# Performance work log

Measured on AMD Instinct MI355X. Metric: run time of the kernel, lower is better.

## Reference

```python
import jax, jax.numpy as jnp
import numpy as np

B, N, D, ATT = 8, 2048, 1024, 128

def setup_inputs() -> dict:
    key = jax.random.key(0)
    k1, k2, k3 = jax.random.split(key, 3)
    s = 1.0 / np.sqrt(D)
    return {
        "x": jax.random.normal(k1, (B, N, D), dtype=jnp.float32),
        "Wf": jax.random.normal(k2, (D, ATT), dtype=jnp.float32) * s,
        "bf": jnp.zeros((ATT,), dtype=jnp.float32),
        "Wg": jax.random.normal(k3, (D, ATT), dtype=jnp.float32) * s,
        "bg": jnp.zeros((ATT,), dtype=jnp.float32),
    }

def reference(x, Wf, bf, Wg, bg):
    # f, g: [B, N, ATT]
    f = jnp.einsum('bnd,da->bna', x, Wf) + bf
    g = jnp.einsum('bnd,da->bna', x, Wg) + bg
    # unscaled attention logits [B, N, N]
    att = jnp.einsum('bna,bma->bnm', f, g)
    att = jax.nn.softmax(att, axis=-1)
    # NOTE: original multiplies attention with x (not h); h branch is dead code.
    out = jnp.einsum('bnm,bmd->bnd', att, x)
    return out + x  # residual=True
```

## Files before the change

kernel.cpp:

```cpp
#include <hip/hip_runtime.h>
#include <hip/hip_fp16.h>


#define B_ 8
#define N_ 2048
#define D_ 1024
#define A_ 128

typedef _Float16 half8v  __attribute__((ext_vector_type(8)));
typedef _Float16 half4v  __attribute__((ext_vector_type(4)));
typedef float    floatx4 __attribute__((ext_vector_type(4)));

__device__ __forceinline__ floatx4 mfma32(half8v a, half8v b, floatx4 c) {
#if defined(__HIP_DEVICE_COMPILE__)
    return __builtin_amdgcn_mfma_f32_16x16x32_f16(a, b, c, 0, 0, 0);
#else
    return c;
#endif
}

__global__ __launch_bounds__(256) void xpose_kernel(
    const float* __restrict__ x, _Float16* __restrict__ xT)
{
    __shared__ __align__(16) _Float16 ts[64][80];
    const int n0 = blockIdx.x * 64, d0 = blockIdx.y * 64, b = blockIdx.z;
    const int t = threadIdx.x;
#pragma unroll
    for (int s = 0; s < 4; ++s) {
        int idx = t + 256 * s;
        int nl = idx >> 4, c4 = idx & 15;
        float4 v = ((const float4*)(x + ((size_t)(b * N_ + n0 + nl)) * D_ + d0))[c4];
        ts[c4 * 4 + 0][nl] = (_Float16)v.x;
        ts[c4 * 4 + 1][nl] = (_Float16)v.y;
        ts[c4 * 4 + 2][nl] = (_Float16)v.z;
        ts[c4 * 4 + 3][nl] = (_Float16)v.w;
    }
    __syncthreads();
#pragma unroll
    for (int s = 0; s < 2; ++s) {
        int idx = t + 256 * s;
        int dl = idx >> 3, c = idx & 7;
        *(uint4*)&xT[((size_t)b * D_ + d0 + dl) * N_ + n0 + c * 8] =
            *(const uint4*)&ts[dl][c * 8];
    }
}

__global__ __launch_bounds__(256) void wprep_kernel(
    const float* __restrict__ Wf, const float* __restrict__ Wg,
    _Float16* __restrict__ whT)
{
    __shared__ __align__(16) _Float16 ts[64][72];
    const int k0 = blockIdx.x * 64, c0 = blockIdx.y * 64;
    const float* W = blockIdx.z ? Wg : Wf;
    _Float16* dst = whT + (size_t)blockIdx.z * A_ * D_;
    const int t = threadIdx.x;
#pragma unroll
    for (int s = 0; s < 4; ++s) {
        int idx = t + 256 * s;
        int kl = idx >> 4, c4 = idx & 15;
        float4 v = *(const float4*)&W[(size_t)(k0 + kl) * A_ + c0 + c4 * 4];
        ts[c4 * 4 + 0][kl] = (_Float16)v.x;
        ts[c4 * 4 + 1][kl] = (_Float16)v.y;
        ts[c4 * 4 + 2][kl] = (_Float16)v.z;
        ts[c4 * 4 + 3][kl] = (_Float16)v.w;
    }
    __syncthreads();
#pragma unroll
    for (int s = 0; s < 2; ++s) {
        int idx = t + 256 * s;
        int cl = idx >> 3, ch = idx & 7;
        *(uint4*)&dst[(size_t)(c0 + cl) * D_ + k0 + ch * 8] =
            *(const uint4*)&ts[cl][ch * 8];
    }
}

__global__ __launch_bounds__(256) void fgmm_kernel(
    const float* __restrict__ x, const _Float16* __restrict__ whT,
    const float* __restrict__ bfv, const float* __restrict__ bgv,
    _Float16* __restrict__ fh, _Float16* __restrict__ gh)
{
    __shared__ __align__(16) _Float16 xs[64 * 40];
    __shared__ __align__(16) _Float16 wt[256 * 40];
    const int row0 = blockIdx.x * 64;
    const int t = threadIdx.x;
    const int w = t >> 6, lane = t & 63, quad = lane >> 4, l16 = lane & 15;
    const int wr  = (w >> 1) * 32;
    const int wch = (w & 1);

    float4 xRf[2];
    uint4  wR[4];
#define FG_LOAD_TILE(K0)                                                      \
    {                                                                         \
        _Pragma("unroll")                                                     \
        for (int s = 0; s < 2; ++s) {                                         \
            int idx = t + 256 * s;                                            \
            int r = idx >> 3, k4 = idx & 7;                                   \
            xRf[s] = *(const float4*)&x[(size_t)(row0 + r) * D_ + (K0) + k4 * 4]; \
        }                                                                     \
        _Pragma("unroll")                                                     \
        for (int s = 0; s < 4; ++s) {                                         \
            int idx = t + 256 * s;                                            \
            int c = idx >> 2, k8 = idx & 3;                                   \
            wR[s] = *(const uint4*)&whT[(size_t)c * D_ + (K0) + k8 * 8];      \
        }                                                                     \
    }

    FG_LOAD_TILE(0)

    floatx4 acc[2][8];
#pragma unroll
    for (int ms = 0; ms < 2; ++ms)
#pragma unroll
        for (int nt = 0; nt < 8; ++nt)
            acc[ms][nt] = (floatx4){0.f, 0.f, 0.f, 0.f};

    for (int kt = 0; kt < 32; ++kt) {
        __syncthreads();
#pragma unroll
        for (int s = 0; s < 2; ++s) {
            int idx = t + 256 * s;
            int r = idx >> 3, k4 = idx & 7;
            half4v h = {(_Float16)xRf[s].x, (_Float16)xRf[s].y,
                        (_Float16)xRf[s].z, (_Float16)xRf[s].w};
            *(half4v*)&xs[r * 40 + k4 * 4] = h;
        }
#pragma unroll
        for (int s = 0; s < 4; ++s) {
            int idx = t + 256 * s;
            int c = idx >> 2, k8 = idx & 3;
            *(uint4*)&wt[c * 40 + k8 * 8] = wR[s];
        }
        __syncthreads();
        if (kt < 31) FG_LOAD_TILE((kt + 1) * 32)

        half8v a0 = *(const half8v*)&xs[(wr + l16) * 40 + quad * 8];
        half8v a1 = *(const half8v*)&xs[(wr + 16 + l16) * 40 + quad * 8];
#pragma unroll
        for (int nt = 0; nt < 8; ++nt) {
            half8v bfr = *(const half8v*)&wt[(wch * 128 + nt * 16 + l16) * 40 + quad * 8];
            acc[0][nt] = mfma32(a0, bfr, acc[0][nt]);
            acc[1][nt] = mfma32(a1, bfr, acc[1][nt]);
        }
    }

    _Float16* dst = wch ? gh : fh;
    const float* bias = wch ? bgv : bfv;
#pragma unroll
    for (int nt = 0; nt < 8; ++nt) {
        int col = nt * 16 + l16;
        float bv = bias[col];
#pragma unroll
        for (int ms = 0; ms < 2; ++ms)
#pragma unroll
            for (int rg = 0; rg < 4; ++rg) {
                int row = row0 + wr + ms * 16 + quad * 4 + rg;
                dst[(size_t)row * A_ + col] = (_Float16)(acc[ms][nt][rg] + bv);
            }
    }
}

__global__ __launch_bounds__(256, 2) void attn_kernel(
    const float* __restrict__ x, const _Float16* __restrict__ f,
    const _Float16* __restrict__ g, const _Float16* __restrict__ xT,
    float* __restrict__ out)
{
    __shared__ __align__(16) _Float16 gS[2][32 * 136];
    __shared__ __align__(16) _Float16 xTs[2][256 * 40];

    const int dch = blockIdx.x;
    const int nt  = blockIdx.y;
    const int b   = blockIdx.z;
    const int tid = threadIdx.x;
    const int wave = tid >> 6, lane = tid & 63;
    const int quad = lane >> 4, l16 = lane & 15;
    const int d0 = dch * 256;
    const int qbase = nt * 128 + wave * 32;

    half8v fb[2][4];
#pragma unroll
    for (int it = 0; it < 2; ++it)
#pragma unroll
        for (int kc = 0; kc < 4; ++kc)
            fb[it][kc] = *(const half8v*)(f +
                ((size_t)(b * N_ + qbase + it * 16 + l16)) * A_ + kc * 32 + quad * 8);

    uint4 gR[2];
    uint2 xR[8];
#define AT_LOAD_TILE(M0)                                                      \
    {                                                                         \
        _Pragma("unroll")                                                     \
        for (int s = 0; s < 2; ++s) {                                         \
            int idx = tid + 256 * s;                                          \
            int r = idx >> 4, c = idx & 15;                                   \
            gR[s] = *(const uint4*)(g + ((size_t)(b * N_ + (M0) + r)) * A_ + c * 8); \
        }                                                                     \
        _Pragma("unroll")                                                     \
        for (int s = 0; s < 8; ++s) {                                         \
            int idx = tid + 256 * s;                                          \
            int rr = idx >> 3, p = idx & 7;                                   \
            xR[s] = *(const uint2*)(xT + ((size_t)b * D_ + d0 + rr) * N_ + (M0) + p * 4); \
        }                                                                     \
    }

#define AT_COMMIT(BUF)                                                        \
    {                                                                         \
        _Pragma("unroll")                                                     \
        for (int s = 0; s < 2; ++s) {                                         \
            int idx = tid + 256 * s;                                          \
            int r = idx >> 4, c = idx & 15;                                   \
            int slot = ((r >> 2) & 1) * 16 + ((r >> 3) & 3) * 4 + (r & 3);    \
            *(uint4*)&gS[BUF][slot * 136 + c * 8] = gR[s];                    \
        }                                                                     \
        _Pragma("unroll")                                                     \
        for (int s = 0; s < 8; ++s) {                                         \
            int idx = tid + 256 * s;                                          \
            int rr = idx >> 3, p = idx & 7;                                   \
            *(uint2*)&xTs[BUF][rr * 40 + p * 4] = xR[s];                      \
        }                                                                     \
    }

    floatx4 acc[2][16];
#pragma unroll
    for (int it = 0; it < 2; ++it)
#pragma unroll
        for (int dt = 0; dt < 16; ++dt)
            acc[it][dt] = (floatx4){0.f, 0.f, 0.f, 0.f};
    float m_i[2]    = {-3.0e38f, -3.0e38f};
    float l_part[2] = {0.f, 0.f};

    AT_LOAD_TILE(0)
    AT_COMMIT(0)
    __syncthreads();
    AT_LOAD_TILE(32)

    for (int t = 0; t < 64; ++t) {
        const int cur = t & 1;
        if (t < 63) AT_COMMIT(cur ^ 1)
        if (t < 62) AT_LOAD_TILE((t + 2) * 32)

        floatx4 sc[2][2];
#pragma unroll
        for (int fr = 0; fr < 2; ++fr)
#pragma unroll
            for (int it = 0; it < 2; ++it)
                sc[fr][it] = (floatx4){0.f, 0.f, 0.f, 0.f};
        __builtin_amdgcn_s_setprio(1);
#pragma unroll
        for (int kc = 0; kc < 4; ++kc) {
            half8v ga0 = *(const half8v*)&gS[cur][(l16     ) * 136 + kc * 32 + quad * 8];
            half8v ga1 = *(const half8v*)&gS[cur][(l16 + 16) * 136 + kc * 32 + quad * 8];
            sc[0][0] = mfma32(ga0, fb[0][kc], sc[0][0]);
            sc[0][1] = mfma32(ga0, fb[1][kc], sc[0][1]);
            sc[1][0] = mfma32(ga1, fb[0][kc], sc[1][0]);
            sc[1][1] = mfma32(ga1, fb[1][kc], sc[1][1]);
        }
        __builtin_amdgcn_s_setprio(0);

        float tm[2];
#pragma unroll
        for (int it = 0; it < 2; ++it) {
            float t0 = fmaxf(fmaxf(sc[0][it][0], sc[0][it][1]),
                             fmaxf(sc[0][it][2], sc[0][it][3]));
            float t1 = fmaxf(fmaxf(sc[1][it][0], sc[1][it][1]),
                             fmaxf(sc[1][it][2], sc[1][it][3]));
            float tv = fmaxf(t0, t1);
            tv = fmaxf(tv, __shfl_xor(tv, 16));
            tv = fmaxf(tv, __shfl_xor(tv, 32));
            tm[it] = tv;
        }
        bool needl = (tm[0] > m_i[0] + 8.0f) || (tm[1] > m_i[1] + 8.0f);
        if (__any(needl)) {
            float alpha[2];
#pragma unroll
            for (int it = 0; it < 2; ++it) {
                float mnew = fmaxf(m_i[it], tm[it]);
                alpha[it] = __expf(m_i[it] - mnew);
                m_i[it] = mnew;
                l_part[it] *= alpha[it];
            }
            float ar[2][4];
#pragma unroll
            for (int it = 0; it < 2; ++it)
#pragma unroll
                for (int r = 0; r < 4; ++r)
                    ar[it][r] = __shfl(alpha[it], quad * 4 + r);
#pragma unroll
            for (int it = 0; it < 2; ++it)
#pragma unroll
                for (int dt = 0; dt < 16; ++dt)
#pragma unroll
                    for (int r = 0; r < 4; ++r)
                        acc[it][dt][r] *= ar[it][r];
        }

        half8v pa[2];
#pragma unroll
        for (int it = 0; it < 2; ++it) {
            float e0 = __expf(sc[0][it][0] - m_i[it]);
            float e1 = __expf(sc[0][it][1] - m_i[it]);
            float e2 = __expf(sc[0][it][2] - m_i[it]);
            float e3 = __expf(sc[0][it][3] - m_i[it]);
            float e4 = __expf(sc[1][it][0] - m_i[it]);
            float e5 = __expf(sc[1][it][1] - m_i[it]);
            float e6 = __expf(sc[1][it][2] - m_i[it]);
            float e7 = __expf(sc[1][it][3] - m_i[it]);
            l_part[it] += ((e0 + e1) + (e2 + e3)) + ((e4 + e5) + (e6 + e7));
            pa[it] = (half8v){(_Float16)e0, (_Float16)e1, (_Float16)e2,
                              (_Float16)e3, (_Float16)e4, (_Float16)e5,
                              (_Float16)e6, (_Float16)e7};
        }

        __builtin_amdgcn_s_setprio(1);
#pragma unroll
        for (int dt = 0; dt < 16; ++dt) {
            half8v xb = *(const half8v*)&xTs[cur][(dt * 16 + l16) * 40 + quad * 8];
            acc[0][dt] = mfma32(pa[0], xb, acc[0][dt]);
            acc[1][dt] = mfma32(pa[1], xb, acc[1][dt]);
        }
        __builtin_amdgcn_s_setprio(0);

        __syncthreads();
    }

    float l_i[2];
#pragma unroll
    for (int it = 0; it < 2; ++it) {
        float rs = l_part[it];
        rs += __shfl_xor(rs, 16);
        rs += __shfl_xor(rs, 32);
        l_i[it] = rs;
    }
    float linv[2][4];
#pragma unroll
    for (int it = 0; it < 2; ++it)
#pragma unroll
        for (int r = 0; r < 4; ++r)
            linv[it][r] = 1.0f / __shfl(l_i[it], quad * 4 + r);

#pragma unroll
    for (int it = 0; it < 2; ++it)
#pragma unroll
        for (int r = 0; r < 4; ++r) {
            const size_t rowoff =
                ((size_t)(b * N_ + qbase + it * 16 + quad * 4 + r)) * D_ + d0;
#pragma unroll
            for (int dt = 0; dt < 16; ++dt) {
                int col = dt * 16 + l16;
                out[rowoff + col] = fmaf(acc[it][dt][r], linv[it][r], x[rowoff + col]);
            }
        }
}

extern "C" void kernel_launch(void* const* d_in, const int* in_sizes, int n_in,
                              void* d_out, int out_size, void* d_ws, size_t ws_size,
                              hipStream_t stream) {
    const float* x   = (const float*)d_in[0];
    const float* Wf  = (const float*)d_in[1];
    const float* bfv = (const float*)d_in[2];
    const float* Wg  = (const float*)d_in[3];
    const float* bgv = (const float*)d_in[4];
    float* out = (float*)d_out;

    _Float16* fh  = (_Float16*)d_ws;
    _Float16* gh  = fh + (size_t)B_ * N_ * A_;
    _Float16* xT  = gh + (size_t)B_ * N_ * A_;
    _Float16* whT = xT + (size_t)B_ * D_ * N_;

    hipLaunchKernelGGL(xpose_kernel, dim3(N_ / 64, D_ / 64, B_), dim3(256), 0, stream,
                       x, xT);
    hipLaunchKernelGGL(wprep_kernel, dim3(D_ / 64, A_ / 64, 2), dim3(256), 0, stream,
                       Wf, Wg, whT);
    hipLaunchKernelGGL(fgmm_kernel, dim3(B_ * N_ / 64), dim3(256), 0, stream,
                       x, whT, bfv, bgv, fh, gh);
    hipLaunchKernelGGL(attn_kernel, dim3(D_ / 256, N_ / 128, B_), dim3(256), 0, stream,
                       x, fh, gh, xT, out);
}
```

Measured before the change: 310.9 us.

## Stage attention tiles via direct global-to-LDS loads and halve d-chunk width

Replaces the register-staged global loads and LDS commits in the attention kernel with global_load_lds direct copies, and uses an XOR swizzle on the g tile in place of padding to avoid bank conflicts. The d-chunk per block shrinks from 256 to 128, which halves accumulators and raises occupancy to 3 blocks per CU. The cost is that the QK^T scores and softmax are recomputed twice as many times across d-chunks, and prefetch depth drops to one tile ahead.

```diff
diff --git a/kernel.cpp b/kernel.cpp
--- a/kernel.cpp
+++ b/kernel.cpp
@@ -16,6 +16,14 @@
     return __builtin_amdgcn_mfma_f32_16x16x32_f16(a, b, c, 0, 0, 0);
 #else
     return c;
+#endif
+}
+
+__device__ __forceinline__ void gload_lds16(const void* gsrc, void* ldst) {
+#if defined(__HIP_DEVICE_COMPILE__)
+    __builtin_amdgcn_global_load_lds(
+        (const __attribute__((address_space(1))) void*)gsrc,
+        (__attribute__((address_space(3))) void*)ldst, 16, 0, 0);
 #endif
 }
 
@@ -159,13 +167,13 @@
     }
 }
 
-__global__ __launch_bounds__(256, 2) void attn_kernel(
+__global__ __launch_bounds__(256, 3) void attn_kernel(
     const float* __restrict__ x, const _Float16* __restrict__ f,
     const _Float16* __restrict__ g, const _Float16* __restrict__ xT,
     float* __restrict__ out)
 {
-    __shared__ __align__(16) _Float16 gS[2][32 * 136];
-    __shared__ __align__(16) _Float16 xTs[2][256 * 40];
+    __shared__ __align__(16) _Float16 gS[2][32 * 128];
+    __shared__ __align__(16) _Float16 xTs[2][128 * 32];
 
     const int dch = blockIdx.x;
     const int nt  = blockIdx.y;
@@ -173,7 +181,7 @@
     const int tid = threadIdx.x;
     const int wave = tid >> 6, lane = tid & 63;
     const int quad = lane >> 4, l16 = lane & 15;
-    const int d0 = dch * 256;
+    const int d0 = dch * 128;
     const int qbase = nt * 128 + wave * 32;
 
     half8v fb[2][4];
@@ -184,59 +192,41 @@
             fb[it][kc] = *(const half8v*)(f +
                 ((size_t)(b * N_ + qbase + it * 16 + l16)) * A_ + kc * 32 + quad * 8);
 
-    uint4 gR[2];
-    uint2 xR[8];
-#define AT_LOAD_TILE(M0)                                                      \
+#define AT_STAGE(BUF, M0)                                                     \
     {                                                                         \
         _Pragma("unroll")                                                     \
         for (int s = 0; s < 2; ++s) {                                         \
-            int idx = tid + 256 * s;                                          \
-            int r = idx >> 4, c = idx & 15;                                   \
-            gR[s] = *(const uint4*)(g + ((size_t)(b * N_ + (M0) + r)) * A_ + c * 8); \
+            int idx = s * 256 + tid;                                          \
+            int rsl = idx >> 4, c = idx & 15;                                 \
+            int j  = ((rsl >> 2) & 3) * 8 + ((rsl >> 4) & 1) * 4 + (rsl & 3); \
+            int cc = c ^ (rsl & 7);                                           \
+            gload_lds16(g + ((size_t)(b * N_ + (M0) + j)) * A_ + cc * 8,      \
+                        &gS[BUF][(s * 256 + wave * 64) * 8]);                 \
         }                                                                     \
         _Pragma("unroll")                                                     \
-        for (int s = 0; s < 8; ++s) {                                         \
-            int idx = tid + 256 * s;                                          \
-            int rr = idx >> 3, p = idx & 7;                                   \
-            xR[s] = *(const uint2*)(xT + ((size_t)b * D_ + d0 + rr) * N_ + (M0) + p * 4); \
+        for (int s = 0; s < 2; ++s) {                                         \
+            int idx = s * 256 + tid;                                          \
+            int rr = idx >> 2, p = idx & 3;                                   \
+            gload_lds16(xT + ((size_t)b * D_ + d0 + rr) * N_ + (M0) + p * 8,  \
+                        &xTs[BUF][(s * 256 + wave * 64) * 8]);                \
         }                                                                     \
     }
 
-#define AT_COMMIT(BUF)                                                        \
-    {                                                                         \
-        _Pragma("unroll")                                                     \
-        for (int s = 0; s < 2; ++s) {                                         \
-            int idx = tid + 256 * s;                                          \
-            int r = idx >> 4, c = idx & 15;                                   \
-            int slot = ((r >> 2) & 1) * 16 + ((r >> 3) & 3) * 4 + (r & 3);    \
-            *(uint4*)&gS[BUF][slot * 136 + c * 8] = gR[s];                    \
-        }                                                                     \
-        _Pragma("unroll")                                                     \
-        for (int s = 0; s < 8; ++s) {                                         \
-            int idx = tid + 256 * s;                                          \
-            int rr = idx >> 3, p = idx & 7;                                   \
-            *(uint2*)&xTs[BUF][rr * 40 + p * 4] = xR[s];                      \
-        }                                                                     \
-    }
-
-    floatx4 acc[2][16];
+    floatx4 acc[2][8];
 #pragma unroll
     for (int it = 0; it < 2; ++it)
 #pragma unroll
-        for (int dt = 0; dt < 16; ++dt)
+        for (int dt = 0; dt < 8; ++dt)
             acc[it][dt] = (floatx4){0.f, 0.f, 0.f, 0.f};
     float m_i[2]    = {-3.0e38f, -3.0e38f};
     float l_part[2] = {0.f, 0.f};
 
-    AT_LOAD_TILE(0)
-    AT_COMMIT(0)
+    AT_STAGE(0, 0)
     __syncthreads();
-    AT_LOAD_TILE(32)
 
     for (int t = 0; t < 64; ++t) {
         const int cur = t & 1;
-        if (t < 63) AT_COMMIT(cur ^ 1)
-        if (t < 62) AT_LOAD_TILE((t + 2) * 32)
+        if (t < 63) AT_STAGE(cur ^ 1, (t + 1) * 32)
 
         floatx4 sc[2][2];
 #pragma unroll
@@ -247,8 +237,9 @@
         __builtin_amdgcn_s_setprio(1);
 #pragma unroll
         for (int kc = 0; kc < 4; ++kc) {
-            half8v ga0 = *(const half8v*)&gS[cur][(l16     ) * 136 + kc * 32 + quad * 8];
-            half8v ga1 = *(const half8v*)&gS[cur][(l16 + 16) * 136 + kc * 32 + quad * 8];
+            int ch = (((kc * 4 + quad) ^ (l16 & 7)) * 8);
+            half8v ga0 = *(const half8v*)&gS[cur][(l16     ) * 128 + ch];
+            half8v ga1 = *(const half8v*)&gS[cur][(l16 + 16) * 128 + ch];
             sc[0][0] = mfma32(ga0, fb[0][kc], sc[0][0]);
             sc[0][1] = mfma32(ga0, fb[1][kc], sc[0][1]);
             sc[1][0] = mfma32(ga1, fb[0][kc], sc[1][0]);
@@ -287,7 +278,7 @@
 #pragma unroll
             for (int it = 0; it < 2; ++it)
 #pragma unroll
-                for (int dt = 0; dt < 16; ++dt)
+                for (int dt = 0; dt < 8; ++dt)
 #pragma unroll
                     for (int r = 0; r < 4; ++r)
                         acc[it][dt][r] *= ar[it][r];
@@ -312,8 +303,8 @@
 
         __builtin_amdgcn_s_setprio(1);
 #pragma unroll
-        for (int dt = 0; dt < 16; ++dt) {
-            half8v xb = *(const half8v*)&xTs[cur][(dt * 16 + l16) * 40 + quad * 8];
+        for (int dt = 0; dt < 8; ++dt) {
+            half8v xb = *(const half8v*)&xTs[cur][(dt * 16 + l16) * 32 + quad * 8];
             acc[0][dt] = mfma32(pa[0], xb, acc[0][dt]);
             acc[1][dt] = mfma32(pa[1], xb, acc[1][dt]);
         }
@@ -344,7 +335,7 @@
             const size_t rowoff =
                 ((size_t)(b * N_ + qbase + it * 16 + quad * 4 + r)) * D_ + d0;
 #pragma unroll
-            for (int dt = 0; dt < 16; ++dt) {
+            for (int dt = 0; dt < 8; ++dt) {
                 int col = dt * 16 + l16;
                 out[rowoff + col] = fmaf(acc[it][dt][r], linv[it][r], x[rowoff + col]);
             }
@@ -372,6 +363,6 @@
                        Wf, Wg, whT);
     hipLaunchKernelGGL(fgmm_kernel, dim3(B_ * N_ / 64), dim3(256), 0, stream,
                        x, whT, bfv, bgv, fh, gh);
-    hipLaunchKernelGGL(attn_kernel, dim3(D_ / 256, N_ / 128, B_), dim3(256), 0, stream,
+    hipLaunchKernelGGL(attn_kernel, dim3(D_ / 128, N_ / 128, B_), dim3(256), 0, stream,
                        x, fh, gh, xT, out);
 }
```

Measured after the change: 343.8 us. 1.11x slower.
